# Kernel tuning notes

Measured on AMD Instinct MI355X. Metric: run time of the kernel, lower is better.

## Reference

```python
import jax, jax.numpy as jnp
import numpy as np

AUDIO_DIM, SEM_DIM, ATTN_DIM = 512, 768, 128


def setup_inputs() -> dict:
    key = jax.random.key(0)
    ks = jax.random.split(key, 12)
    B, T, T_sem = 8, 4096, 1024
    s = lambda d: 1.0 / np.sqrt(d)
    return {
        "x_ct": jax.random.normal(ks[0], (B, AUDIO_DIM, T), jnp.float32),
        "sem_btd": jax.random.normal(ks[1], (B, T_sem, SEM_DIM), jnp.float32),
        "ln_w": jnp.ones((AUDIO_DIM,), jnp.float32),
        "ln_b": jnp.zeros((AUDIO_DIM,), jnp.float32),
        "Wq": jax.random.normal(ks[2], (AUDIO_DIM, ATTN_DIM), jnp.float32) * s(AUDIO_DIM),
        "bq": jnp.zeros((ATTN_DIM,), jnp.float32),
        "Wk": jax.random.normal(ks[3], (SEM_DIM, ATTN_DIM), jnp.float32) * s(SEM_DIM),
        "bk": jnp.zeros((ATTN_DIM,), jnp.float32),
        "Wv": jax.random.normal(ks[4], (SEM_DIM, ATTN_DIM), jnp.float32) * s(SEM_DIM),
        "bv": jnp.zeros((ATTN_DIM,), jnp.float32),
        "Wo": jax.random.normal(ks[5], (ATTN_DIM, AUDIO_DIM), jnp.float32) * s(ATTN_DIM),
        "bo": jnp.zeros((AUDIO_DIM,), jnp.float32),
    }


def _layernorm(x, w, b, eps=1e-5):
    mu = jnp.mean(x, axis=-1, keepdims=True)
    var = jnp.mean(jnp.square(x - mu), axis=-1, keepdims=True)
    return (x - mu) * jax.lax.rsqrt(var + eps) * w + b


def reference(x_ct, sem_btd, ln_w, ln_b, Wq, bq, Wk, bk, Wv, bv, Wo, bo):
    # x_ct: [B, C, T] -> [B, T, C]
    x = jnp.swapaxes(x_ct, 1, 2)
    x = _layernorm(x, ln_w, ln_b)
    Q = x @ Wq + bq                      # [B, T, A]
    K = sem_btd @ Wk + bk                # [B, S, A]
    V = sem_btd @ Wv + bv                # [B, S, A]
    scale = ATTN_DIM ** -0.5
    attn = jnp.einsum("bta,bsa->bts", Q, K) * scale
    attn = jax.nn.softmax(attn, axis=-1)  # dropout: eval mode (identity)
    ctx = jnp.einsum("bts,bsa->bta", attn, V)
    delta = ctx @ Wo + bo                # [B, T, C]
    return jnp.swapaxes(delta, 1, 2)     # [B, C, T]
```

## Files before the change

### kernel.cpp

```cpp
#include <hip/hip_runtime.h>
#include <hip/hip_bf16.h>
#include <math.h>

#define BATCH 8
#define TDIM 4096
#define SDIM 1024
#define CDIM 512
#define DDIM 768
#define ADIM 128

typedef short s8v __attribute__((ext_vector_type(8)));
typedef float f4v __attribute__((ext_vector_type(4)));

__device__ __forceinline__ short f2bf(float f) {
    unsigned u = __float_as_uint(f);
    u += 0x7fffu + ((u >> 16) & 1u);
    return (short)(u >> 16);
}
__device__ __forceinline__ float bf2f(short s) {
    return __uint_as_float(((unsigned)(unsigned short)s) << 16);
}
__device__ __forceinline__ f4v mfma16(s8v a, s8v b, f4v c) {
    return __builtin_amdgcn_mfma_f32_16x16x32_bf16(a, b, c, 0, 0, 0);
}

__global__ __launch_bounds__(256) void prep_w(
    const float* __restrict__ Wq, const float* __restrict__ Wk,
    const float* __restrict__ Wv, const float* __restrict__ Wo,
    const float* __restrict__ lnw, const float* __restrict__ lnb,
    const float* __restrict__ bq,
    short* __restrict__ WqT, short* __restrict__ WkT,
    short* __restrict__ WvT, short* __restrict__ WoT,
    float* __restrict__ uq, float* __restrict__ vq)
{
    __shared__ float su[2][128], sv[2][128];
    int gid = blockIdx.x * 256 + threadIdx.x;
    {
        int k = gid >> 7, n = gid & 127;
        WqT[n * 512 + k] = f2bf(Wq[gid] * lnw[k]);
    }
    #pragma unroll
    for (int i = 0; i < 2; ++i) {
        int e = gid + i * 65536;
        if (e < 98304) {
            int k = e >> 7, n = e & 127;
            WkT[n * 768 + k] = f2bf(Wk[e]);
            WvT[n * 768 + k] = f2bf(Wv[e]);
        }
    }
    {
        int k = gid >> 9, c = gid & 511;
        WoT[c * 128 + k] = f2bf(Wo[gid]);
    }
    if (blockIdx.x == 255) {
        int a = threadIdx.x & 127, half = threadIdx.x >> 7;
        float s1 = 0.f, s2 = 0.f;
        #pragma unroll 8
        for (int c = half * 256; c < half * 256 + 256; ++c) {
            float wv = Wq[c * 128 + a];
            s1 += bf2f(f2bf(lnw[c] * wv));
            s2 += lnb[c] * wv;
        }
        su[half][a] = s1; sv[half][a] = s2;
        __syncthreads();
        if (threadIdx.x < 128) {
            uq[a] = su[0][a] + su[1][a];
            vq[a] = sv[0][a] + sv[1][a] + bq[a];
        }
    }
}

__global__ __launch_bounds__(256) void kv_proj(
    const float* __restrict__ sem,
    const short* __restrict__ WkT, const float* __restrict__ bk,
    const short* __restrict__ WvT, const float* __restrict__ bv,
    short* __restrict__ Kb, short* __restrict__ Vb)
{
    __shared__ __align__(16) short sA[32 * 40];
    __shared__ __align__(16) short sW[2][128 * 40];
    const int tid = threadIdx.x, lane = tid & 63, wave = tid >> 6;
    const int ln15 = lane & 15, q = lane >> 4, kq = q * 8;
    const int r0 = blockIdx.x * 32;
    const int b = r0 >> 10, sbase = r0 & 1023;
    const int kv = wave >> 1;
    const int mh = wave & 1;
    const int m  = mh * 16 + ln15;

    f4v acc[8];
    #pragma unroll
    for (int j = 0; j < 8; ++j) acc[j] = (f4v)0.0f;

    const int srow = tid >> 3;
    const int sk4  = (tid & 7) * 4;

    for (int kc = 0; kc < DDIM / 32; ++kc) {
        __syncthreads();
        {
            float4 f = *(const float4*)&sem[(size_t)(r0 + srow) * DDIM + kc * 32 + sk4];
            uint2 pk;
            pk.x = (unsigned short)f2bf(f.x) | ((unsigned)(unsigned short)f2bf(f.y) << 16);
            pk.y = (unsigned short)f2bf(f.z) | ((unsigned)(unsigned short)f2bf(f.w) << 16);
            *(uint2*)&sA[srow * 40 + sk4] = pk;
        }
        #pragma unroll
        for (int i = 0; i < 2; ++i) {
            int idx8 = i * 256 + tid;
            int n = idx8 >> 2, k8 = (idx8 & 3) * 8;
            *(s8v*)&sW[0][n * 40 + k8] = *(const s8v*)&WkT[(size_t)n * 768 + kc * 32 + k8];
            *(s8v*)&sW[1][n * 40 + k8] = *(const s8v*)&WvT[(size_t)n * 768 + kc * 32 + k8];
        }
        __syncthreads();
        s8v a = *(const s8v*)&sA[m * 40 + kq];
        #pragma unroll
        for (int j = 0; j < 8; ++j) {
            s8v bb = *(const s8v*)&sW[kv][(j * 16 + ln15) * 40 + kq];
            acc[j] = mfma16(a, bb, acc[j]);
        }
    }
    const int s_in_b = sbase + mh * 16 + q * 4;
    if (kv == 0) {
        #pragma unroll
        for (int j = 0; j < 8; ++j) {
            int col = j * 16 + ln15;
            float bias = bk[col];
            #pragma unroll
            for (int r = 0; r < 4; ++r)
                Kb[((size_t)b * SDIM + s_in_b + r) * ADIM + col] = f2bf(acc[j][r] + bias);
        }
    } else {
        #pragma unroll
        for (int j = 0; j < 8; ++j) {
            int col = j * 16 + ln15;
            float bias = bv[col];
            uint2 pk;
            pk.x = (unsigned short)f2bf(acc[j][0] + bias) | ((unsigned)(unsigned short)f2bf(acc[j][1] + bias) << 16);
            pk.y = (unsigned short)f2bf(acc[j][2] + bias) | ((unsigned)(unsigned short)f2bf(acc[j][3] + bias) << 16);
            *(uint2*)&Vb[((size_t)b * ADIM + col) * SDIM + s_in_b] = pk;
        }
    }
}

__global__ __launch_bounds__(256, 4) void ln_q(
    const float* __restrict__ x,
    const short* __restrict__ WqT, const float* __restrict__ uq,
    const float* __restrict__ vq, short* __restrict__ Qb)
{
    __shared__ __align__(16) short xt[32 * 512];
    __shared__ __align__(16) float redw[4][32][2];
    const int tid = threadIdx.x, lane = tid & 63, wave = tid >> 6;
    const int ln15 = lane & 15, q = lane >> 4, kq = q * 8;
    const int b = blockIdx.x >> 7;
    const int t0 = (blockIdx.x & 127) * 32;
    const float* xb = x + (size_t)b * CDIM * TDIM;

    const int tq = (tid & 7) * 4;
    const int g  = tid >> 3;
    float ps1[4] = {0.f,0.f,0.f,0.f}, ps2[4] = {0.f,0.f,0.f,0.f};
    #pragma unroll
    for (int i = 0; i < 16; ++i) {
        int c = i * 32 + g;
        float4 f = *(const float4*)&xb[(size_t)c * TDIM + t0 + tq];
        float vv[4] = { f.x, f.y, f.z, f.w };
        int kb = c >> 3, cl = c & 7;
        #pragma unroll
        for (int jj = 0; jj < 4; ++jj) {
            int t = tq + jj;
            ps1[jj] += vv[jj]; ps2[jj] += vv[jj] * vv[jj];
            int swz = ((t >> 2) & 7) | ((t & 3) << 3);
            xt[t * 512 + ((kb ^ swz) * 8) + cl] = f2bf(vv[jj]);
        }
    }
    #pragma unroll
    for (int mk = 8; mk <= 32; mk <<= 1) {
        #pragma unroll
        for (int jj = 0; jj < 4; ++jj) {
            ps1[jj] += __shfl_xor(ps1[jj], mk, 64);
            ps2[jj] += __shfl_xor(ps2[jj], mk, 64);
        }
    }
    if ((lane >> 3) == 0) {
        #pragma unroll
        for (int jj = 0; jj < 4; ++jj) {
            redw[wave][tq + jj][0] = ps1[jj];
            redw[wave][tq + jj][1] = ps2[jj];
        }
    }
    __syncthreads();

    const int mrow = (wave & 1) * 16 + ln15;
    const int jb = (wave >> 1) * 4;
    const int swzm = ((mrow >> 2) & 7) | ((mrow & 3) << 3);
    f4v acc[4];
    #pragma unroll
    for (int j = 0; j < 4; ++j) acc[j] = (f4v)0.0f;
    s8v bbuf[2][4];
    #pragma unroll
    for (int j = 0; j < 4; ++j)
        bbuf[0][j] = *(const s8v*)&WqT[(size_t)((jb + j) * 16 + ln15) * 512 + kq];
    #pragma unroll
    for (int kf = 0; kf < 16; ++kf) {
        const int cur = kf & 1;
        if (kf < 15) {
            #pragma unroll
            for (int j = 0; j < 4; ++j)
                bbuf[cur ^ 1][j] = *(const s8v*)&WqT[(size_t)((jb + j) * 16 + ln15) * 512 + (kf + 1) * 32 + kq];
        }
        s8v a = *(const s8v*)&xt[mrow * 512 + (((kf * 4 + q) ^ swzm) * 8)];
        #pragma unroll
        for (int j = 0; j < 4; ++j)
            acc[j] = mfma16(a, bbuf[cur][j], acc[j]);
    }

    float u4[4], v4[4];
    #pragma unroll
    for (int j = 0; j < 4; ++j) {
        int col = (jb + j) * 16 + ln15;
        u4[j] = uq[col]; v4[j] = vq[col];
    }
    const float scale = 0.08838834764831845f;
    #pragma unroll
    for (int r = 0; r < 4; ++r) {
        int tl = (wave & 1) * 16 + q * 4 + r;
        float s1 = 0.f, s2 = 0.f;
        #pragma unroll
        for (int w = 0; w < 4; ++w) {
            float2 p = *(const float2*)&redw[w][tl][0];
            s1 += p.x; s2 += p.y;
        }
        float mu = s1 * (1.f / 512.f);
        float var = s2 * (1.f / 512.f) - mu * mu;
        float rs = rsqrtf(var + 1e-5f);
        int t = t0 + tl;
        #pragma unroll
        for (int j = 0; j < 4; ++j) {
            float qv = (rs * (acc[j][r] - mu * u4[j]) + v4[j]) * scale;
            Qb[((size_t)b * TDIM + t) * ADIM + ((jb + j) * 16 + ln15)] = f2bf(qv);
        }
    }
}

__global__ __launch_bounds__(256) void attn(
    const short* __restrict__ Qb, const short* __restrict__ Kb,
    const short* __restrict__ Vb, short* __restrict__ Cx)
{
    __shared__ __align__(16) short sK [2][64 * 128];
    __shared__ __align__(16) short sVT[2][128 * 64];
    __shared__ __align__(16) short sP [64 * 64];
    const int tid = threadIdx.x, lane = tid & 63, wave = tid >> 6;
    const int ln15 = lane & 15, q = lane >> 4, kq = q * 8;
    const int b = blockIdx.x >> 6;
    const int t0 = (blockIdx.x & 63) * 64;
    const int m = wave * 16 + ln15;

    const int krow = tid >> 4, kkb = tid & 15;
    const int varow = tid >> 3, vkb = tid & 7;

    s8v qf[4];
    {
        const short* qp = Qb + ((size_t)b * TDIM + t0 + m) * ADIM + kq;
        #pragma unroll
        for (int kc = 0; kc < 4; ++kc) qf[kc] = *(const s8v*)(qp + kc * 32);
    }
    s8v ones;
    #pragma unroll
    for (int j = 0; j < 8; ++j) ones[j] = (short)0x3F80;

    f4v accO[8]; f4v accL = (f4v)0.0f;
    #pragma unroll
    for (int j = 0; j < 8; ++j) accO[j] = (f4v)0.0f;

    const short* Kbase = Kb + (size_t)b * SDIM * ADIM;
    const short* Vbase = Vb + (size_t)b * ADIM * SDIM;
    s8v rk[4], rv[4];

    #pragma unroll
    for (int i = 0; i < 4; ++i) {
        rk[i] = *(const s8v*)(Kbase + (size_t)(i * 16 + krow) * ADIM + kkb * 8);
        rv[i] = *(const s8v*)(Vbase + (size_t)(i * 32 + varow) * SDIM + vkb * 8);
    }
    #pragma unroll
    for (int i = 0; i < 4; ++i) {
        int r = i * 16 + krow;
        *(s8v*)&sK[0][r * 128 + ((kkb ^ (r & 15)) * 8)] = rk[i];
        int a = i * 32 + varow;
        *(s8v*)&sVT[0][a * 64 + ((vkb ^ (a & 7)) * 8)] = rv[i];
    }
    __syncthreads();

    for (int sc = 0; sc < SDIM / 64; ++sc) {
        const int cur = sc & 1;
        if (sc < 15) {
            const int s0n = (sc + 1) * 64;
            #pragma unroll
            for (int i = 0; i < 4; ++i) {
                rk[i] = *(const s8v*)(Kbase + (size_t)(s0n + i * 16 + krow) * ADIM + kkb * 8);
                rv[i] = *(const s8v*)(Vbase + (size_t)(i * 32 + varow) * SDIM + s0n + vkb * 8);
            }
        }
        #pragma unroll
        for (int j = 0; j < 4; ++j) {
            f4v sacc = (f4v)0.0f;
            const int row = j * 16 + ln15;
            #pragma unroll
            for (int kc = 0; kc < 4; ++kc) {
                s8v bb = *(const s8v*)&sK[cur][row * 128 + (((kc * 4 + q) ^ (row & 15)) * 8)];
                sacc = mfma16(qf[kc], bb, sacc);
            }
            #pragma unroll
            for (int r = 0; r < 4; ++r) {
                float ev = __expf(sacc[r]);
                int prow = wave * 16 + q * 4 + r;
                int pcol = j * 16 + ln15;
                sP[prow * 64 + (((pcol >> 3) ^ (prow & 7)) * 8) + (pcol & 7)] = f2bf(ev);
            }
        }
        #pragma unroll
        for (int kc = 0; kc < 2; ++kc) {
            s8v pa = *(const s8v*)&sP[m * 64 + (((kc * 4 + q) ^ (m & 7)) * 8)];
            accL = mfma16(pa, ones, accL);
            #pragma unroll
            for (int j = 0; j < 8; ++j) {
                int a = j * 16 + ln15;
                s8v bb = *(const s8v*)&sVT[cur][a * 64 + (((kc * 4 + q) ^ (a & 7)) * 8)];
                accO[j] = mfma16(pa, bb, accO[j]);
            }
        }
        if (sc < 15) {
            #pragma unroll
            for (int i = 0; i < 4; ++i) {
                int r = i * 16 + krow;
                *(s8v*)&sK[cur ^ 1][r * 128 + ((kkb ^ (r & 15)) * 8)] = rk[i];
                int a = i * 32 + varow;
                *(s8v*)&sVT[cur ^ 1][a * 64 + ((vkb ^ (a & 7)) * 8)] = rv[i];
            }
        }
        __syncthreads();
    }
    #pragma unroll
    for (int r = 0; r < 4; ++r) {
        float rinv = 1.0f / accL[r];
        int t = t0 + wave * 16 + q * 4 + r;
        #pragma unroll
        for (int j = 0; j < 8; ++j) {
            int col = j * 16 + ln15;
            Cx[((size_t)b * TDIM + t) * ADIM + col] = f2bf(accO[j][r] * rinv);
        }
    }
}

__global__ __launch_bounds__(256) void out_proj(
    const short* __restrict__ Cx, const short* __restrict__ WoT,
    const float* __restrict__ bo, float* __restrict__ out)
{
    __shared__ __align__(16) short sCtx[64 * 136];
    __shared__ __align__(16) char  buf[128 * 136 * 2];
    short* sWoT = (short*)buf;
    float* outT = (float*)buf;
    const int tid = threadIdx.x, lane = tid & 63, wave = tid >> 6;
    const int ln15 = lane & 15, q = lane >> 4, kq = q * 8;
    const int b = blockIdx.x >> 8;
    const int rem = blockIdx.x & 255;
    const int t0 = (rem & 63) * 64;
    const int c0 = (rem >> 6) * 128;

    #pragma unroll
    for (int i = 0; i < 4; ++i) {
        int idx8 = i * 256 + tid;
        int row = idx8 >> 4, a8 = (idx8 & 15) * 8;
        *(s8v*)&sCtx[row * 136 + a8] = *(const s8v*)&Cx[((size_t)b * TDIM + t0 + row) * ADIM + a8];
    }
    #pragma unroll
    for (int i = 0; i < 8; ++i) {
        int idx8 = i * 256 + tid;
        int n = idx8 >> 4, k8 = (idx8 & 15) * 8;
        *(s8v*)&sWoT[n * 136 + k8] = *(const s8v*)&WoT[(size_t)(c0 + n) * ADIM + k8];
    }
    __syncthreads();
    f4v acc[8];
    #pragma unroll
    for (int j = 0; j < 8; ++j) acc[j] = (f4v)0.0f;
    const int m = wave * 16 + ln15;
    #pragma unroll
    for (int kc = 0; kc < 4; ++kc) {
        s8v a = *(const s8v*)&sCtx[m * 136 + kc * 32 + kq];
        #pragma unroll
        for (int j = 0; j < 8; ++j) {
            s8v bb = *(const s8v*)&sWoT[(j * 16 + ln15) * 136 + kc * 32 + kq];
            acc[j] = mfma16(a, bb, acc[j]);
        }
    }
    __syncthreads();
    #pragma unroll
    for (int j = 0; j < 8; ++j) {
        int cl = j * 16 + ln15;
        float bias = bo[c0 + cl];
        #pragma unroll
        for (int r = 0; r < 4; ++r) {
            int tl = wave * 16 + q * 4 + r;
            outT[cl * 68 + tl] = acc[j][r] + bias;
        }
    }
    __syncthreads();
    #pragma unroll
    for (int i = 0; i < 8; ++i) {
        int idx4 = i * 256 + tid;
        int c = idx4 >> 4, t4 = (idx4 & 15) * 4;
        float4 v = *(const float4*)&outT[c * 68 + t4];
        *(float4*)&out[((size_t)b * CDIM + c0 + c) * TDIM + t0 + t4] = v;
    }
}

extern "C" void kernel_launch(void* const* d_in, const int* in_sizes, int n_in,
                              void* d_out, int out_size, void* d_ws, size_t ws_size,
                              hipStream_t stream) {
    const float* x   = (const float*)d_in[0];
    const float* sem = (const float*)d_in[1];
    const float* lnw = (const float*)d_in[2];
    const float* lnb = (const float*)d_in[3];
    const float* Wq  = (const float*)d_in[4];
    const float* bq  = (const float*)d_in[5];
    const float* Wk  = (const float*)d_in[6];
    const float* bk  = (const float*)d_in[7];
    const float* Wv  = (const float*)d_in[8];
    const float* bv  = (const float*)d_in[9];
    const float* Wo  = (const float*)d_in[10];
    const float* bo  = (const float*)d_in[11];
    float* out = (float*)d_out;

    short* ws  = (short*)d_ws;
    short* Qb  = ws;
    short* Kb  = Qb  + (size_t)BATCH * TDIM * ADIM;
    short* Vb  = Kb  + (size_t)BATCH * SDIM * ADIM;
    short* Cx  = Vb  + (size_t)BATCH * SDIM * ADIM;
    short* WqT = Cx  + (size_t)BATCH * TDIM * ADIM;
    short* WkT = WqT + 128 * 512;
    short* WvT = WkT + 128 * 768;
    short* WoT = WvT + 128 * 768;
    float* uq  = (float*)(WoT + 512 * 128);
    float* vq  = uq + 128;

    hipLaunchKernelGGL(prep_w,  dim3(256),  dim3(256), 0, stream,
                       Wq, Wk, Wv, Wo, lnw, lnb, bq, WqT, WkT, WvT, WoT, uq, vq);
    hipLaunchKernelGGL(kv_proj, dim3(256),  dim3(256), 0, stream, sem, WkT, bk, WvT, bv, Kb, Vb);
    hipLaunchKernelGGL(ln_q,    dim3(1024), dim3(256), 0, stream, x, WqT, uq, vq, Qb);
    hipLaunchKernelGGL(attn,    dim3(512),  dim3(256), 0, stream, Qb, Kb, Vb, Cx);
    hipLaunchKernelGGL(out_proj,dim3(2048), dim3(256), 0, stream, Cx, WoT, bo, out);
}
```

Baseline: 264.4 us.

## Pipeline ln_q over K chunks with double-buffered x and async Wq LDS loads

Restructures the LayerNorm+Q-projection kernel so the 512-channel reduction runs in 8 chunks of 64. Each chunk's x tile and Wq tile are prefetched into double-buffered shared memory while the previous chunk's MFMAs execute, with Wq staged through global_load_lds. Wq is pre-swizzled in prep_w into a chunked, XOR-swizzled layout to suit this. The intent is to overlap the global loads of x and Wq with compute instead of loading all of x first. In exchange it adds a barrier per chunk and lowers the occupancy hint from 4 to 3 blocks per SM.

```diff
diff --git a/kernel.cpp b/kernel.cpp
--- a/kernel.cpp
+++ b/kernel.cpp
@@ -22,6 +22,11 @@
 }
 __device__ __forceinline__ f4v mfma16(s8v a, s8v b, f4v c) {
     return __builtin_amdgcn_mfma_f32_16x16x32_bf16(a, b, c, 0, 0, 0);
+}
+__device__ __forceinline__ void gl_lds16(const short* g, short* l) {
+    __builtin_amdgcn_global_load_lds(
+        (const __attribute__((address_space(1))) unsigned int*)g,
+        (__attribute__((address_space(3))) unsigned int*)l, 16, 0, 0);
 }
 
 __global__ __launch_bounds__(256) void prep_w(
@@ -37,7 +42,8 @@
     int gid = blockIdx.x * 256 + threadIdx.x;
     {
         int k = gid >> 7, n = gid & 127;
-        WqT[n * 512 + k] = f2bf(Wq[gid] * lnw[k]);
+        int idx = (k >> 6) * 8192 + n * 64 + ((((k >> 3) & 7) ^ (n & 7)) * 8) + (k & 7);
+        WqT[idx] = f2bf(Wq[gid] * lnw[k]);
     }
     #pragma unroll
     for (int i = 0; i < 2; ++i) {
@@ -140,76 +146,107 @@
     }
 }
 
-__global__ __launch_bounds__(256, 4) void ln_q(
+__global__ __launch_bounds__(256, 3) void ln_q(
     const float* __restrict__ x,
-    const short* __restrict__ WqT, const float* __restrict__ uq,
+    const short* __restrict__ WqI, const float* __restrict__ uq,
     const float* __restrict__ vq, short* __restrict__ Qb)
 {
-    __shared__ __align__(16) short xt[32 * 512];
+    __shared__ __align__(16) short sX[2][32 * 72];
+    __shared__ __align__(16) short sW[2][64 * 128];
     __shared__ __align__(16) float redw[4][32][2];
     const int tid = threadIdx.x, lane = tid & 63, wave = tid >> 6;
     const int ln15 = lane & 15, q = lane >> 4, kq = q * 8;
     const int b = blockIdx.x >> 7;
     const int t0 = (blockIdx.x & 127) * 32;
-    const float* xb = x + (size_t)b * CDIM * TDIM;
-
-    const int tq = (tid & 7) * 4;
-    const int g  = tid >> 3;
-    float ps1[4] = {0.f,0.f,0.f,0.f}, ps2[4] = {0.f,0.f,0.f,0.f};
-    #pragma unroll
-    for (int i = 0; i < 16; ++i) {
-        int c = i * 32 + g;
-        float4 f = *(const float4*)&xb[(size_t)c * TDIM + t0 + tq];
-        float vv[4] = { f.x, f.y, f.z, f.w };
-        int kb = c >> 3, cl = c & 7;
+    const float* xb = x + (size_t)b * CDIM * TDIM + t0;
+
+    const int cc  = tid >> 2;
+    const int tlo = (tid & 3) * 4;
+    const int thi = 16 + tlo;
+    const int wb  = wave * 64;
+
+    float ps1[8] = {0,0,0,0,0,0,0,0}, ps2[8] = {0,0,0,0,0,0,0,0};
+    const int mh = wave & 1, jb = (wave >> 1) * 4;
+    const int mrow = mh * 16 + ln15;
+    f4v acc[4];
+    #pragma unroll
+    for (int j = 0; j < 4; ++j) acc[j] = (f4v)0.0f;
+
+    float4 f0 = *(const float4*)&xb[(size_t)cc * TDIM + tlo];
+    float4 f1 = *(const float4*)&xb[(size_t)cc * TDIM + thi];
+    #pragma unroll
+    for (int i = 0; i < 4; ++i) {
+        int ii = i * 256 + wb;
+        gl_lds16(&WqI[(size_t)(ii + lane) * 8], &sW[0][ii * 8]);
+    }
+    {
+        float v0[4] = {f0.x, f0.y, f0.z, f0.w};
+        float v1[4] = {f1.x, f1.y, f1.z, f1.w};
         #pragma unroll
         for (int jj = 0; jj < 4; ++jj) {
-            int t = tq + jj;
-            ps1[jj] += vv[jj]; ps2[jj] += vv[jj] * vv[jj];
-            int swz = ((t >> 2) & 7) | ((t & 3) << 3);
-            xt[t * 512 + ((kb ^ swz) * 8) + cl] = f2bf(vv[jj]);
-        }
-    }
-    #pragma unroll
-    for (int mk = 8; mk <= 32; mk <<= 1) {
-        #pragma unroll
-        for (int jj = 0; jj < 4; ++jj) {
+            ps1[jj] += v0[jj];     ps2[jj] += v0[jj] * v0[jj];
+            ps1[4+jj] += v1[jj];   ps2[4+jj] += v1[jj] * v1[jj];
+            sX[0][(tlo + jj) * 72 + cc] = f2bf(v0[jj]);
+            sX[0][(thi + jj) * 72 + cc] = f2bf(v1[jj]);
+        }
+    }
+    __syncthreads();
+
+    for (int kc = 0; kc < 8; ++kc) {
+        const int cur = kc & 1;
+        if (kc < 7) {
+            const size_t cb = (size_t)(kc + 1) * 64;
+            f0 = *(const float4*)&xb[(cb + cc) * TDIM + tlo];
+            f1 = *(const float4*)&xb[(cb + cc) * TDIM + thi];
+            const short* wch = WqI + (size_t)(kc + 1) * 8192;
+            #pragma unroll
+            for (int i = 0; i < 4; ++i) {
+                int ii = i * 256 + wb;
+                gl_lds16(&wch[(size_t)(ii + lane) * 8], &sW[cur ^ 1][ii * 8]);
+            }
+        }
+        #pragma unroll
+        for (int kk = 0; kk < 2; ++kk) {
+            s8v a = *(const s8v*)&sX[cur][mrow * 72 + kk * 32 + kq];
+            #pragma unroll
+            for (int j = 0; j < 4; ++j) {
+                int n = (jb + j) * 16 + ln15;
+                s8v bb = *(const s8v*)&sW[cur][n * 64 + (((kk * 4 + q) ^ (n & 7)) * 8)];
+                acc[j] = mfma16(a, bb, acc[j]);
+            }
+        }
+        if (kc < 7) {
+            float v0[4] = {f0.x, f0.y, f0.z, f0.w};
+            float v1[4] = {f1.x, f1.y, f1.z, f1.w};
+            #pragma unroll
+            for (int jj = 0; jj < 4; ++jj) {
+                ps1[jj] += v0[jj];     ps2[jj] += v0[jj] * v0[jj];
+                ps1[4+jj] += v1[jj];   ps2[4+jj] += v1[jj] * v1[jj];
+                sX[cur ^ 1][(tlo + jj) * 72 + cc] = f2bf(v0[jj]);
+                sX[cur ^ 1][(thi + jj) * 72 + cc] = f2bf(v1[jj]);
+            }
+        }
+        __syncthreads();
+    }
+
+    #pragma unroll
+    for (int mk = 4; mk <= 32; mk <<= 1) {
+        #pragma unroll
+        for (int jj = 0; jj < 8; ++jj) {
             ps1[jj] += __shfl_xor(ps1[jj], mk, 64);
             ps2[jj] += __shfl_xor(ps2[jj], mk, 64);
         }
     }
-    if ((lane >> 3) == 0) {
+    if (lane < 4) {
         #pragma unroll
         for (int jj = 0; jj < 4; ++jj) {
-            redw[wave][tq + jj][0] = ps1[jj];
-            redw[wave][tq + jj][1] = ps2[jj];
-        }
-    }
-    __syncthreads();
-
-    const int mrow = (wave & 1) * 16 + ln15;
-    const int jb = (wave >> 1) * 4;
-    const int swzm = ((mrow >> 2) & 7) | ((mrow & 3) << 3);
-    f4v acc[4];
-    #pragma unroll
-    for (int j = 0; j < 4; ++j) acc[j] = (f4v)0.0f;
-    s8v bbuf[2][4];
-    #pragma unroll
-    for (int j = 0; j < 4; ++j)
-        bbuf[0][j] = *(const s8v*)&WqT[(size_t)((jb + j) * 16 + ln15) * 512 + kq];
-    #pragma unroll
-    for (int kf = 0; kf < 16; ++kf) {
-        const int cur = kf & 1;
-        if (kf < 15) {
-            #pragma unroll
-            for (int j = 0; j < 4; ++j)
-                bbuf[cur ^ 1][j] = *(const s8v*)&WqT[(size_t)((jb + j) * 16 + ln15) * 512 + (kf + 1) * 32 + kq];
-        }
-        s8v a = *(const s8v*)&xt[mrow * 512 + (((kf * 4 + q) ^ swzm) * 8)];
-        #pragma unroll
-        for (int j = 0; j < 4; ++j)
-            acc[j] = mfma16(a, bbuf[cur][j], acc[j]);
-    }
+            redw[wave][tlo + jj][0] = ps1[jj];
+            redw[wave][tlo + jj][1] = ps2[jj];
+            redw[wave][thi + jj][0] = ps1[4 + jj];
+            redw[wave][thi + jj][1] = ps2[4 + jj];
+        }
+    }
+    __syncthreads();
 
     float u4[4], v4[4];
     #pragma unroll
@@ -220,7 +257,7 @@
     const float scale = 0.08838834764831845f;
     #pragma unroll
     for (int r = 0; r < 4; ++r) {
-        int tl = (wave & 1) * 16 + q * 4 + r;
+        int tl = mh * 16 + q * 4 + r;
         float s1 = 0.f, s2 = 0.f;
         #pragma unroll
         for (int w = 0; w < 4; ++w) {
```

Result: faster. 250.1 us (-5.4%).
